# Kernel optimization log

Hardware: AMD Instinct MI355X
Metric: run time of the kernel (lower is better)

## Reference

```python
import jax, jax.numpy as jnp
import numpy as np
import math

B, S, H = 2, 2048, 2048
NH, HD = 16, 64  # head_dim = H // (2*NH)
LAMBDA_INIT = 0.5


def setup_inputs() -> dict:
    key = jax.random.key(0)
    ks = jax.random.split(key, 6)
    std = 1.0 / math.sqrt(H)
    hidden_states = jax.random.normal(ks[0], (B, S, H), dtype=jnp.float32)
    # Linear weights stored as [in, out] (x @ W)
    Wq = jax.random.normal(ks[1], (H, 2 * NH * HD), dtype=jnp.float32) * std
    Wk = jax.random.normal(ks[2], (H, 2 * NH * HD), dtype=jnp.float32) * std
    Wv = jax.random.normal(ks[3], (H, NH * HD), dtype=jnp.float32) * std
    Wo = jax.random.normal(ks[4], (NH * HD, H), dtype=jnp.float32) * (1.0 / math.sqrt(NH * HD))
    lambda_param = jnp.log(jnp.asarray(1.0 / math.tanh(LAMBDA_INIT), dtype=jnp.float32))
    # causal additive mask, (B, 1, S, S)
    causal = jnp.tril(jnp.ones((S, S), dtype=bool))
    attention_mask = jnp.where(causal, 0.0, jnp.finfo(jnp.float32).min)[None, None]
    attention_mask = jnp.broadcast_to(attention_mask, (B, 1, S, S))
    return {"hidden_states": hidden_states, "attention_mask": attention_mask,
            "Wq": Wq, "Wk": Wk, "Wv": Wv, "Wo": Wo, "lambda_param": lambda_param}


def reference(hidden_states, attention_mask, Wq, Wk, Wv, Wo, lambda_param):
    bsz, q_len, _ = hidden_states.shape
    scaling = HD ** -0.5

    q_all = (hidden_states @ Wq).reshape(bsz, q_len, 2 * NH, HD).transpose(0, 2, 1, 3)
    k_all = (hidden_states @ Wk).reshape(bsz, q_len, 2 * NH, HD).transpose(0, 2, 1, 3)
    v = (hidden_states @ Wv).reshape(bsz, q_len, NH, HD).transpose(0, 2, 1, 3)
    q1, q2 = q_all[:, :NH], q_all[:, NH:]
    k1, k2 = k_all[:, :NH], k_all[:, NH:]

    lam = jnp.tanh(jax.nn.softplus(lambda_param))
    scores1 = jnp.einsum('bhqd,bhkd->bhqk', q1, k1) * scaling
    scores2 = jnp.einsum('bhqd,bhkd->bhqk', q2, k2) * scaling
    attn_scores = scores1 - lam * scores2 + attention_mask
    attn_weights = jax.nn.softmax(attn_scores.astype(jnp.float32), axis=-1).astype(q1.dtype)

    attn_out = jnp.einsum('bhqk,bhkd->bhqd', attn_weights, v)
    attn_out = attn_out.transpose(0, 2, 1, 3).reshape(bsz, q_len, NH * HD)
    return attn_out @ Wo
```

## Files before the change

kernel.cpp:

```cpp
#include <hip/hip_runtime.h>
#include <hip/hip_bf16.h>

#define B_ 2
#define S_ 2048
#define H_ 2048
#define NH_ 16
#define HD_ 64
#define DQ_ 2048
#define DV_ 1024
#define QKS_ 4096

using bf16x8 = __attribute__((ext_vector_type(8))) __bf16;
using f32x4  = __attribute__((ext_vector_type(4))) float;

typedef __attribute__((address_space(1))) unsigned int u32g;
typedef __attribute__((address_space(3))) unsigned int u32l;

__device__ __forceinline__ void gload_lds16(const __bf16* g, __bf16* l) {
  __builtin_amdgcn_global_load_lds((u32g*)g, (u32l*)l, 16, 0, 0);
}

__device__ __forceinline__ int swz(int row, int colb, int strideB) {
  return row * strideB + (colb ^ (((row ^ (row >> 3)) & 7) << 4));
}
__device__ __forceinline__ int fxor(int row) { return (row ^ (row >> 3)) & 7; }

__device__ __forceinline__ unsigned int pk2(float a, float b) {
  __bf16 ba = (__bf16)a, bb = (__bf16)b;
  unsigned short ua, ub;
  __builtin_memcpy(&ua, &ba, 2);
  __builtin_memcpy(&ub, &bb, 2);
  return (unsigned int)ua | ((unsigned int)ub << 16);
}


__global__ __launch_bounds__(256) void cast_hidden(const float* __restrict__ in,
                                                   __bf16* __restrict__ out, int n) {
  int i = (blockIdx.x * 256 + threadIdx.x) * 8;
  if (i >= n) return;
  float4 a = *reinterpret_cast<const float4*>(in + i);
  float4 b = *reinterpret_cast<const float4*>(in + i + 4);
  bf16x8 o;
  o[0] = (__bf16)a.x; o[1] = (__bf16)a.y; o[2] = (__bf16)a.z; o[3] = (__bf16)a.w;
  o[4] = (__bf16)b.x; o[5] = (__bf16)b.y; o[6] = (__bf16)b.z; o[7] = (__bf16)b.w;
  *reinterpret_cast<bf16x8*>(out + i) = o;
}

__global__ __launch_bounds__(256) void transpose_cast(const float* __restrict__ in,
                                                      __bf16* __restrict__ out, int R, int C) {
  __shared__ float tile[32][33];
  int tx = threadIdx.x & 31, ty = threadIdx.x >> 5;
  int c0 = blockIdx.x * 32, r0 = blockIdx.y * 32;
  for (int i = 0; i < 32; i += 8)
    tile[ty + i][tx] = in[(size_t)(r0 + ty + i) * C + c0 + tx];
  __syncthreads();
  for (int i = 0; i < 32; i += 8)
    out[(size_t)(c0 + ty + i) * R + r0 + tx] = (__bf16)tile[tx][ty + i];
}


template <typename OutT>
__global__ __launch_bounds__(256) void gemm_bt(const __bf16* __restrict__ A,
                                               const __bf16* __restrict__ Bt,
                                               OutT* __restrict__ C,
                                               int M, int N, int K) {
  __shared__ __bf16 As[2][128 * 32];
  __shared__ __bf16 Bs[2][128 * 32];
  const int nx = gridDim.x;
  int id = blockIdx.y * nx + blockIdx.x;
  const int cpx = (nx * gridDim.y) >> 3;
  id = (id & 7) * cpx + (id >> 3);
  const int bm = id / nx, bn = id % nx;

  const int tid = threadIdx.x;
  const int wid = tid >> 6, lane = tid & 63;
  const int wm = wid >> 1, wn = wid & 1;
  const int g = lane >> 4, c = lane & 15;

  f32x4 acc[4][4] = {};
  const __bf16* Abase = A + (size_t)(bm * 128) * K;
  const __bf16* Bbase = Bt + (size_t)(bn * 128) * K;
  const int srow = wid * 16 + (lane >> 2);
  const int scol = (lane & 3) * 8;
  const int nk = K >> 5;

  auto stage = [&](int p, int kt) {
    int k0 = kt * 32;
    gload_lds16(Abase + (size_t)srow * K + k0 + scol,        &As[p][(wid * 16) * 32]);
    gload_lds16(Abase + (size_t)(srow + 64) * K + k0 + scol, &As[p][(64 + wid * 16) * 32]);
    gload_lds16(Bbase + (size_t)srow * K + k0 + scol,        &Bs[p][(wid * 16) * 32]);
    gload_lds16(Bbase + (size_t)(srow + 64) * K + k0 + scol, &Bs[p][(64 + wid * 16) * 32]);
  };

  stage(0, 0);
  stage(1, 1);

  for (int kt = 0; kt < nk; ++kt) {
    const int p = kt & 1;
    if (kt + 1 < nk) {
      asm volatile("s_waitcnt vmcnt(4)" ::: "memory");
    } else {
      asm volatile("s_waitcnt vmcnt(0)" ::: "memory");
    }
    __builtin_amdgcn_s_barrier();
    __builtin_amdgcn_sched_barrier(0);

    bf16x8 af[4], bfv[4];
#pragma unroll
    for (int i = 0; i < 4; ++i)
      af[i] = *reinterpret_cast<const bf16x8*>(&As[p][(wm * 64 + i * 16 + c) * 32 + g * 8]);
#pragma unroll
    for (int i = 0; i < 4; ++i)
      bfv[i] = *reinterpret_cast<const bf16x8*>(&Bs[p][(wn * 64 + i * 16 + c) * 32 + g * 8]);
#pragma unroll
    for (int m = 0; m < 4; ++m)
#pragma unroll
      for (int n = 0; n < 4; ++n)
        acc[m][n] = __builtin_amdgcn_mfma_f32_16x16x32_bf16(af[m], bfv[n], acc[m][n], 0, 0, 0);

    __builtin_amdgcn_sched_barrier(0);
    __builtin_amdgcn_s_barrier();
    if (kt + 2 < nk) stage(p, kt + 2);
  }

#pragma unroll
  for (int m = 0; m < 4; ++m)
#pragma unroll
    for (int n = 0; n < 4; ++n)
#pragma unroll
      for (int r = 0; r < 4; ++r) {
        int row = bm * 128 + wm * 64 + m * 16 + g * 4 + r;
        int col = bn * 128 + wn * 64 + n * 16 + c;
        float v = acc[m][n][r];
        if constexpr (sizeof(OutT) == 2)
          C[(size_t)row * N + col] = (OutT)(__bf16)v;
        else
          C[(size_t)row * N + col] = v;
      }
}


template <typename OutT>
__global__ __launch_bounds__(512, 2) void gemm256(const __bf16* __restrict__ A,
                                                  const __bf16* __restrict__ Bt,
                                                  OutT* __restrict__ C,
                                                  int M, int N, int K) {
  __shared__ __bf16 As[2][256 * 64];
  __shared__ __bf16 Bs[2][256 * 64];
  const int nx = gridDim.x;
  int id = blockIdx.y * nx + blockIdx.x;
  const int cpx = (nx * gridDim.y) >> 3;
  id = (id & 7) * cpx + (id >> 3);
  const int bm = id / nx, bn = id % nx;

  const int tid = threadIdx.x;
  const int wid = tid >> 6, lane = tid & 63;
  const int wm = wid >> 2, wn = wid & 3;
  const int g = lane >> 4, c = lane & 15;

  f32x4 acc[8][4] = {};
  bf16x8 af[4][2];
  bf16x8 bfv[4][2];
  const __bf16* Abase = A + (size_t)(bm * 256) * K;
  const __bf16* Bbase = Bt + (size_t)(bn * 256) * K;
  const int niter = K >> 7;

  auto stageA = [&](int p, int half, int kt) {
#pragma unroll
    for (int j = 0; j < 2; ++j) {
      int row = half * 128 + j * 64 + wid * 8 + (lane >> 3);
      int gc = (lane & 7) ^ (row & 7);
      gload_lds16(Abase + (size_t)row * K + kt * 64 + gc * 8,
                  &As[p][(half * 128 + j * 64 + wid * 8) * 64]);
    }
  };
  auto stageB = [&](int p, int half, int kt) {
#pragma unroll
    for (int j = 0; j < 2; ++j) {
      int row = half * 128 + j * 64 + wid * 8 + (lane >> 3);
      int gc = (lane & 7) ^ (row & 7);
      gload_lds16(Bbase + (size_t)row * K + kt * 64 + gc * 8,
                  &Bs[p][(half * 128 + j * 64 + wid * 8) * 64]);
    }
  };
  auto readA = [&](int p, int m, int kk) -> bf16x8 {
    int row = wm * 128 + m * 16 + c;
    int ch = (kk * 4 + g) ^ (row & 7);
    return *reinterpret_cast<const bf16x8*>(&As[p][row * 64 + ch * 8]);
  };
  auto readB = [&](int p, int n, int kk) -> bf16x8 {
    int row = wn * 64 + n * 16 + c;
    int ch = (kk * 4 + g) ^ (row & 7);
    return *reinterpret_cast<const bf16x8*>(&Bs[p][row * 64 + ch * 8]);
  };
  auto quad = [&](int mb, int nb) {
    __builtin_amdgcn_s_setprio(1);
#pragma unroll
    for (int mi = 0; mi < 4; ++mi)
#pragma unroll
      for (int ni = 0; ni < 2; ++ni)
#pragma unroll
        for (int kk = 0; kk < 2; ++kk)
          acc[mb + mi][nb + ni] = __builtin_amdgcn_mfma_f32_16x16x32_bf16(
              af[mi][kk], bfv[nb + ni][kk], acc[mb + mi][nb + ni], 0, 0, 0);
    __builtin_amdgcn_s_setprio(0);
  };
#define BAR1_LGKM()  __builtin_amdgcn_s_barrier(); \
    asm volatile("s_waitcnt lgkmcnt(0)" ::: "memory"); \
    __builtin_amdgcn_sched_barrier(0)
#define BAR2()  __builtin_amdgcn_sched_barrier(0); __builtin_amdgcn_s_barrier()

  stageA(0, 0, 0); stageA(0, 1, 0);
  stageB(0, 0, 0); stageB(0, 1, 0);
  stageB(1, 0, 1); stageB(1, 1, 1);
  asm volatile("s_waitcnt vmcnt(0)" ::: "memory");
  __builtin_amdgcn_s_barrier();

  for (int i = 0; i < niter; ++i) {
    const int t1 = 2 * i + 1;
    const bool more = (i + 1 < niter);
#pragma unroll
    for (int mi = 0; mi < 4; ++mi) { af[mi][0] = readA(0, mi, 0); af[mi][1] = readA(0, mi, 1); }
#pragma unroll
    for (int ni = 0; ni < 2; ++ni) { bfv[ni][0] = readB(0, ni, 0); bfv[ni][1] = readB(0, ni, 1); }
    stageA(1, 0, t1);
    BAR1_LGKM(); quad(0, 0); BAR2();
#pragma unroll
    for (int ni = 2; ni < 4; ++ni) { bfv[ni][0] = readB(0, ni, 0); bfv[ni][1] = readB(0, ni, 1); }
    stageA(1, 1, t1);
    BAR1_LGKM(); quad(0, 2); BAR2();
#pragma unroll
    for (int mi = 0; mi < 4; ++mi) { af[mi][0] = readA(0, 4 + mi, 0); af[mi][1] = readA(0, 4 + mi, 1); }
    if (more) stageB(0, 0, t1 + 1);
    BAR1_LGKM(); quad(4, 0); BAR2();
    if (more) {
      stageB(0, 1, t1 + 1);
      asm volatile("s_waitcnt vmcnt(4)" ::: "memory");
    } else {
      asm volatile("s_waitcnt vmcnt(0)" ::: "memory");
    }
    __builtin_amdgcn_s_barrier();
    __builtin_amdgcn_sched_barrier(0);
    quad(4, 2); BAR2();
#pragma unroll
    for (int mi = 0; mi < 4; ++mi) { af[mi][0] = readA(1, mi, 0); af[mi][1] = readA(1, mi, 1); }
#pragma unroll
    for (int ni = 0; ni < 2; ++ni) { bfv[ni][0] = readB(1, ni, 0); bfv[ni][1] = readB(1, ni, 1); }
    if (more) stageA(0, 0, t1 + 1);
    BAR1_LGKM(); quad(0, 0); BAR2();
#pragma unroll
    for (int ni = 2; ni < 4; ++ni) { bfv[ni][0] = readB(1, ni, 0); bfv[ni][1] = readB(1, ni, 1); }
    if (more) stageA(0, 1, t1 + 1);
    BAR1_LGKM(); quad(0, 2); BAR2();
#pragma unroll
    for (int mi = 0; mi < 4; ++mi) { af[mi][0] = readA(1, 4 + mi, 0); af[mi][1] = readA(1, 4 + mi, 1); }
    if (more) stageB(1, 0, t1 + 2);
    BAR1_LGKM(); quad(4, 0); BAR2();
    if (more) {
      stageB(1, 1, t1 + 2);
      asm volatile("s_waitcnt vmcnt(4)" ::: "memory");
    } else {
      asm volatile("s_waitcnt vmcnt(0)" ::: "memory");
    }
    __builtin_amdgcn_s_barrier();
    __builtin_amdgcn_sched_barrier(0);
    quad(4, 2); BAR2();
  }
#undef BAR1_LGKM
#undef BAR2

#pragma unroll
  for (int m = 0; m < 8; ++m)
#pragma unroll
    for (int n = 0; n < 4; ++n)
#pragma unroll
      for (int r = 0; r < 4; ++r) {
        int row = bm * 256 + wm * 128 + m * 16 + g * 4 + r;
        int col = bn * 256 + wn * 64 + n * 16 + c;
        float v = acc[m][n][r];
        if constexpr (sizeof(OutT) == 2)
          C[(size_t)row * N + col] = (OutT)(__bf16)v;
        else
          C[(size_t)row * N + col] = v;
      }
}


__global__ __launch_bounds__(256, 2) void diffattn(const __bf16* __restrict__ QK,
                                                   const __bf16* __restrict__ V,
                                                   __bf16* __restrict__ OpA,
                                                   __bf16* __restrict__ OpB,
                                                   float* __restrict__ ml,
                                                   const float* __restrict__ lambda_param) {
  __shared__ __bf16 Ks[2][64 * 128];
  __shared__ __bf16 Vs[2][64 * 64];

  const int y = blockIdx.y;
  const int qt = ((y >> 4) & 1) ? blockIdx.x : (gridDim.x - 1 - blockIdx.x);
  const int bh = y >> 1;
  const int half = y & 1;
  const int b = bh >> 4, h = bh & 15;
  const int tid = threadIdx.x;
  const int w = tid >> 6, lane = tid & 63;
  const int g = lane >> 4, c = lane & 15;
  const float NEG_INF = -__builtin_inff();

  const int srcA = c + 32 * (g & 1);
  const int srcB = srcA + 16;
  const bool hiF = ((g >> 1) & 1) != 0;

  const float lam = tanhf(log1pf(__expf(lambda_param[0])));
  const float L2E = 1.4426950408889634f;
  const float sc1 = 0.125f * L2E;
  const float sc2 = -lam * 0.125f * L2E;

  bf16x8 qf[2][4];
#pragma unroll
  for (int fr = 0; fr < 2; ++fr) {
    int qrow = qt * 128 + w * 32 + fr * 16 + c;
    const __bf16* qbase = QK + (size_t)(b * S_ + qrow) * QKS_;
#pragma unroll
    for (int kk = 0; kk < 4; ++kk) {
      int d = kk * 32 + g * 8;
      const __bf16* src = (d < 64) ? (qbase + h * 64 + d)
                                   : (qbase + DV_ + h * 64 + (d - 64));
      float s = (d < 64) ? sc1 : sc2;
      bf16x8 raw = *reinterpret_cast<const bf16x8*>(src);
      bf16x8 ov;
#pragma unroll
      for (int i = 0; i < 8; ++i) ov[i] = (__bf16)((float)raw[i] * s);
      qf[fr][kk] = ov;
    }
  }

  f32x4 acc[2][4] = {};
  float mrow[2], lrow[2];
#pragma unroll
  for (int fr = 0; fr < 2; ++fr) { mrow[fr] = -1e30f; lrow[fr] = 0.f; }

  const int kt0 = half ? (qt + 1) : 0;
  const int kt1 = half ? (2 * qt + 2) : (qt + 1);

  auto stageK = [&](int p, int kt) {
#pragma unroll
    for (int j = 0; j < 4; ++j) {
      int row = w * 16 + j * 4 + (lane >> 4);
      int gc = (lane & 15) ^ fxor(row);
      int s = kt * 64 + row;
      const __bf16* kbase = QK + (size_t)(b * S_ + s) * QKS_ + 2048;
      const __bf16* src = (gc < 8) ? (kbase + h * 64 + gc * 8)
                                   : (kbase + DV_ + h * 64 + (gc - 8) * 8);
      gload_lds16(src, &Ks[p][(w * 16 + j * 4) * 128]);
    }
  };
  auto loadV = [&](int kt, bf16x8* vv) {
#pragma unroll
    for (int j = 0; j < 2; ++j) {
      int flat = tid + j * 256;
      int kv = flat >> 3;
      int d = (flat & 7) * 8;
      vv[j] = *reinterpret_cast<const bf16x8*>(
          V + (size_t)(b * S_ + kt * 64 + kv) * DV_ + h * 64 + d);
    }
  };
  auto scatterV = [&](int p, const bf16x8* vv) {
    char* VsB = (char*)Vs[p];
#pragma unroll
    for (int j = 0; j < 2; ++j) {
      int flat = tid + j * 256;
      int kv = flat >> 3;
      int d = (flat & 7) * 8;
#pragma unroll
      for (int i = 0; i < 8; ++i)
        *reinterpret_cast<__bf16*>(VsB + swz(d + i, kv * 2, 128)) = vv[j][i];
    }
  };

  {
    stageK(0, kt0);
    bf16x8 vv[2];
    loadV(kt0, vv);
    scatterV(0, vv);
    __syncthreads();
  }

  for (int kt = kt0; kt < kt1; ++kt) {
    const int p = (kt - kt0) & 1;
    const bool pre = (kt + 1 < kt1);
    bf16x8 vv[2];
    if (pre) {
      stageK(p ^ 1, kt + 1);
      loadV(kt + 1, vv);
    }

    f32x4 sc[2][4] = {};
    char* KsB = (char*)Ks[p];
    __builtin_amdgcn_s_setprio(1);
#pragma unroll
    for (int f = 0; f < 4; ++f)
#pragma unroll
      for (int kk = 0; kk < 4; ++kk) {
        bf16x8 kf = *reinterpret_cast<const bf16x8*>(
            KsB + swz(f * 16 + c, (kk * 32 + g * 8) * 2, 256));
        sc[0][f] = __builtin_amdgcn_mfma_f32_16x16x32_bf16(kf, qf[0][kk], sc[0][f], 0, 0, 0);
        sc[1][f] = __builtin_amdgcn_mfma_f32_16x16x32_bf16(kf, qf[1][kk], sc[1][f], 0, 0, 0);
      }
    __builtin_amdgcn_s_setprio(0);

    const int dz = kt - 2 * qt;
    char* VsB = (char*)Vs[p];
#pragma unroll
    for (int fr = 0; fr < 2; ++fr) {
      const int wq = w * 32 + fr * 16 + c;
      float pmax = NEG_INF;
      if (dz >= 0) {
#pragma unroll
        for (int f = 0; f < 4; ++f)
#pragma unroll
          for (int r = 0; r < 4; ++r) {
            float s = sc[fr][f][r];
            if (dz * 64 + f * 16 + g * 4 + r > wq) s = NEG_INF;
            sc[fr][f][r] = s;
            pmax = fmaxf(pmax, s);
          }
      } else {
#pragma unroll
        for (int f = 0; f < 4; ++f)
#pragma unroll
          for (int r = 0; r < 4; ++r)
            pmax = fmaxf(pmax, sc[fr][f][r]);
      }

      if (!__all(pmax - mrow[fr] <= 8.0f)) {
        pmax = fmaxf(pmax, __shfl_xor(pmax, 16, 64));
        pmax = fmaxf(pmax, __shfl_xor(pmax, 32, 64));
        float mnew = fmaxf(mrow[fr], pmax);
        float pscl = __builtin_amdgcn_exp2f(mrow[fr] - mnew);
        mrow[fr] = mnew;
        lrow[fr] *= pscl;
#pragma unroll
        for (int n = 0; n < 4; ++n)
#pragma unroll
          for (int r = 0; r < 4; ++r)
            acc[fr][n][r] *= pscl;
      }

      float rs = 0.f;
#pragma unroll
      for (int f = 0; f < 4; ++f)
#pragma unroll
        for (int r = 0; r < 4; ++r) {
          float pv = __builtin_amdgcn_exp2f(sc[fr][f][r] - mrow[fr]);
          sc[fr][f][r] = pv;
          rs += pv;
        }
      lrow[fr] += rs;

      unsigned int pk[4][2];
#pragma unroll
      for (int f = 0; f < 4; ++f) {
        pk[f][0] = pk2(sc[fr][f][0], sc[fr][f][1]);
        pk[f][1] = pk2(sc[fr][f][2], sc[fr][f][3]);
      }

      __builtin_amdgcn_s_setprio(1);
#pragma unroll
      for (int kc = 0; kc < 2; ++kc) {
        const int fA = kc * 2, fB = kc * 2 + 1;
        unsigned int a0 = __shfl((int)pk[fA][0], srcA, 64);
        unsigned int a1 = __shfl((int)pk[fA][1], srcA, 64);
        unsigned int a2 = __shfl((int)pk[fA][0], srcB, 64);
        unsigned int a3 = __shfl((int)pk[fA][1], srcB, 64);
        unsigned int b0 = __shfl((int)pk[fB][0], srcA, 64);
        unsigned int b1 = __shfl((int)pk[fB][1], srcA, 64);
        unsigned int b2 = __shfl((int)pk[fB][0], srcB, 64);
        unsigned int b3 = __shfl((int)pk[fB][1], srcB, 64);
        union { unsigned int u[4]; bf16x8 v; } pu;
        pu.u[0] = hiF ? b0 : a0;
        pu.u[1] = hiF ? b1 : a1;
        pu.u[2] = hiF ? b2 : a2;
        pu.u[3] = hiF ? b3 : a3;
#pragma unroll
        for (int n = 0; n < 4; ++n) {
          bf16x8 vf = *reinterpret_cast<const bf16x8*>(
              VsB + swz(n * 16 + c, (kc * 32 + g * 8) * 2, 128));
          acc[fr][n] = __builtin_amdgcn_mfma_f32_16x16x32_bf16(vf, pu.v, acc[fr][n], 0, 0, 0);
        }
      }
      __builtin_amdgcn_s_setprio(0);
    }

    if (pre) scatterV(p ^ 1, vv);
    __syncthreads();
  }

  __bf16* Op = half ? OpB : OpA;
#pragma unroll
  for (int fr = 0; fr < 2; ++fr) {
    int q = qt * 128 + w * 32 + fr * 16 + c;
#pragma unroll
    for (int n = 0; n < 4; ++n)
#pragma unroll
      for (int r = 0; r < 4; ++r) {
        int d = n * 16 + g * 4 + r;
        Op[((size_t)bh * 64 + d) * S_ + q] = (__bf16)acc[fr][n][r];
      }
    float lt = lrow[fr];
    lt += __shfl_xor(lt, 16, 64);
    lt += __shfl_xor(lt, 32, 64);
    if (g == 0) {
      float2 v;
      v.x = mrow[fr];
      v.y = lt;
      *reinterpret_cast<float2*>(&ml[((size_t)(half * 32 + bh) * S_ + q) * 2]) = v;
    }
  }
}


__global__ __launch_bounds__(256) void merge_halves(const __bf16* __restrict__ OpA,
                                                    const __bf16* __restrict__ OpB,
                                                    const float* __restrict__ ml,
                                                    __bf16* __restrict__ AO) {
  __shared__ __bf16 tile[64][72];
  __shared__ float wAB[64][2];
  const int bh = blockIdx.y;
  const int q0 = blockIdx.x * 64;
  const int b = bh >> 4, h = bh & 15;
  const int t = threadIdx.x;

  if (t < 64) {
    float2 a2 = *reinterpret_cast<const float2*>(&ml[((size_t)bh * S_ + q0 + t) * 2]);
    float2 b2 = *reinterpret_cast<const float2*>(&ml[((size_t)(32 + bh) * S_ + q0 + t) * 2]);
    float m = fmaxf(a2.x, b2.x);
    float wA = __builtin_amdgcn_exp2f(a2.x - m);
    float wB = __builtin_amdgcn_exp2f(b2.x - m);
    float inv = 1.0f / (a2.y * wA + b2.y * wB);
    wAB[t][0] = wA * inv;
    wAB[t][1] = wB * inv;
  }
  __syncthreads();

#pragma unroll
  for (int i = 0; i < 2; ++i) {
    int d = (t >> 3) + i * 32;
    int qc = (t & 7) * 8;
    size_t base = ((size_t)bh * 64 + d) * S_ + q0 + qc;
    bf16x8 oa = *reinterpret_cast<const bf16x8*>(OpA + base);
    bf16x8 ob = *reinterpret_cast<const bf16x8*>(OpB + base);
#pragma unroll
    for (int j = 0; j < 8; ++j)
      tile[d][qc + j] = (__bf16)((float)oa[j] * wAB[qc + j][0] + (float)ob[j] * wAB[qc + j][1]);
  }
  __syncthreads();

#pragma unroll
  for (int i = 0; i < 2; ++i) {
    int ql = (t >> 3) + i * 32;
    int dc = (t & 7) * 8;
    bf16x8 o;
#pragma unroll
    for (int j = 0; j < 8; ++j) o[j] = tile[dc + j][ql];
    *reinterpret_cast<bf16x8*>(AO + (size_t)(b * S_ + q0 + ql) * DV_ + h * 64 + dc) = o;
  }
}


extern "C" void kernel_launch(void* const* d_in, const int* in_sizes, int n_in,
                              void* d_out, int out_size, void* d_ws, size_t ws_size,
                              hipStream_t stream) {
  const float* hidden = (const float*)d_in[0];
  const float* Wq = (const float*)d_in[2];
  const float* Wk = (const float*)d_in[3];
  const float* Wv = (const float*)d_in[4];
  const float* Wo = (const float*)d_in[5];
  const float* lambda_param = (const float*)d_in[6];
  float* out = (float*)d_out;

  char* ws = (char*)d_ws;
  size_t off = 0;
  auto alloc = [&](size_t bytes) {
    void* p = ws + off;
    off += (bytes + 255) & ~(size_t)255;
    return p;
  };
  const int M = B_ * S_;
  __bf16* hidb = (__bf16*)alloc((size_t)M * H_ * 2);
  __bf16* TB   = (__bf16*)alloc((size_t)QKS_ * H_ * 2);
  __bf16* QKa  = (__bf16*)alloc((size_t)M * QKS_ * 2);
  __bf16* Va   = (__bf16*)((char*)TB + 4u * 1024 * 1024);
  __bf16* AO   = Va;
  float*  mlb  = (float*)((char*)TB + 12u * 1024 * 1024);
  __bf16* OpA  = hidb;
  __bf16* OpB  = hidb + (size_t)M * DV_;
  (void)ws_size; (void)in_sizes; (void)n_in; (void)out_size;

  int nh = M * H_;
  cast_hidden<<<nh / (256 * 8), 256, 0, stream>>>(hidden, hidb, nh);

  transpose_cast<<<dim3(DQ_ / 32, H_ / 32), 256, 0, stream>>>(Wq, TB, H_, DQ_);
  transpose_cast<<<dim3(DQ_ / 32, H_ / 32), 256, 0, stream>>>(Wk, TB + (size_t)DQ_ * H_, H_, DQ_);
  gemm256<__bf16><<<dim3(QKS_ / 256, M / 256), 512, 0, stream>>>(hidb, TB, QKa, M, QKS_, H_);

  transpose_cast<<<dim3(DV_ / 32, H_ / 32), 256, 0, stream>>>(Wv, TB, H_, DV_);
  gemm_bt<__bf16><<<dim3(DV_ / 128, M / 128), 256, 0, stream>>>(hidb, TB, Va, M, DV_, H_);

  diffattn<<<dim3(S_ / 128, B_ * NH_ * 2), 256, 0, stream>>>(QKa, Va, OpA, OpB, mlb, lambda_param);

  transpose_cast<<<dim3(H_ / 32, DV_ / 32), 256, 0, stream>>>(Wo, TB, DV_, H_);
  merge_halves<<<dim3(S_ / 64, B_ * NH_), 256, 0, stream>>>(OpA, OpB, mlb, AO);

  gemm_bt<float><<<dim3(H_ / 128, M / 128), 256, 0, stream>>>(AO, TB, out, M, H_, DV_);
}
```

Measured before the change: 238.4 us.

## Compute softmax row sums via MFMA with ones vector and hoist V fragment loads

```diff
diff --git a/kernel.cpp b/kernel.cpp
--- a/kernel.cpp
+++ b/kernel.cpp
@@ -314,6 +314,10 @@
   const float sc1 = 0.125f * L2E;
   const float sc2 = -lam * 0.125f * L2E;
 
+  bf16x8 ones;
+#pragma unroll
+  for (int i = 0; i < 8; ++i) ones[i] = (__bf16)1.0f;
+
   bf16x8 qf[2][4];
 #pragma unroll
   for (int fr = 0; fr < 2; ++fr) {
@@ -407,8 +411,16 @@
       }
     __builtin_amdgcn_s_setprio(0);
 
+    char* VsB = (char*)Vs[p];
+    bf16x8 vfr[2][4];
+#pragma unroll
+    for (int kc = 0; kc < 2; ++kc)
+#pragma unroll
+      for (int n = 0; n < 4; ++n)
+        vfr[kc][n] = *reinterpret_cast<const bf16x8*>(
+            VsB + swz(n * 16 + c, (kc * 32 + g * 8) * 2, 128));
+
     const int dz = kt - 2 * qt;
-    char* VsB = (char*)Vs[p];
 #pragma unroll
     for (int fr = 0; fr < 2; ++fr) {
       const int wq = w * 32 + fr * 16 + c;
@@ -445,16 +457,11 @@
             acc[fr][n][r] *= pscl;
       }
 
-      float rs = 0.f;
 #pragma unroll
       for (int f = 0; f < 4; ++f)
 #pragma unroll
-        for (int r = 0; r < 4; ++r) {
-          float pv = __builtin_amdgcn_exp2f(sc[fr][f][r] - mrow[fr]);
-          sc[fr][f][r] = pv;
-          rs += pv;
-        }
-      lrow[fr] += rs;
+        for (int r = 0; r < 4; ++r)
+          sc[fr][f][r] = __builtin_amdgcn_exp2f(sc[fr][f][r] - mrow[fr]);
 
       unsigned int pk[4][2];
 #pragma unroll
@@ -463,6 +470,7 @@
         pk[f][1] = pk2(sc[fr][f][2], sc[fr][f][3]);
       }
 
+      f32x4 rs = {};
       __builtin_amdgcn_s_setprio(1);
 #pragma unroll
       for (int kc = 0; kc < 2; ++kc) {
@@ -480,14 +488,13 @@
         pu.u[1] = hiF ? b1 : a1;
         pu.u[2] = hiF ? b2 : a2;
         pu.u[3] = hiF ? b3 : a3;
-#pragma unroll
-        for (int n = 0; n < 4; ++n) {
-          bf16x8 vf = *reinterpret_cast<const bf16x8*>(
-              VsB + swz(n * 16 + c, (kc * 32 + g * 8) * 2, 128));
-          acc[fr][n] = __builtin_amdgcn_mfma_f32_16x16x32_bf16(vf, pu.v, acc[fr][n], 0, 0, 0);
-        }
+        rs = __builtin_amdgcn_mfma_f32_16x16x32_bf16(ones, pu.v, rs, 0, 0, 0);
+#pragma unroll
+        for (int n = 0; n < 4; ++n)
+          acc[fr][n] = __builtin_amdgcn_mfma_f32_16x16x32_bf16(vfr[kc][n], pu.v, acc[fr][n], 0, 0, 0);
       }
       __builtin_amdgcn_s_setprio(0);
+      lrow[fr] += rs[0];
     }
 
     if (pre) scatterV(p ^ 1, vv);
@@ -505,13 +512,10 @@
         int d = n * 16 + g * 4 + r;
         Op[((size_t)bh * 64 + d) * S_ + q] = (__bf16)acc[fr][n][r];
       }
-    float lt = lrow[fr];
-    lt += __shfl_xor(lt, 16, 64);
-    lt += __shfl_xor(lt, 32, 64);
     if (g == 0) {
       float2 v;
       v.x = mrow[fr];
-      v.y = lt;
+      v.y = lrow[fr];
       *reinterpret_cast<float2*>(&ml[((size_t)(half * 32 + bh) * S_ + q) * 2]) = v;
     }
   }
```

After: 237.6 us. Within noise of the previous version (-0.3%).
